# Performance work log

Measured on AMD Instinct MI355X. Metric: run time of the kernel, lower is better.

## Reference

```python
import jax, jax.numpy as jnp
import numpy as np
from jax import lax

NSTEPS = 4
STEPSIZE = 0.1


def setup_inputs() -> dict:
    key = jax.random.key(0)
    k1, k2, k3, k4 = jax.random.split(key, 4)
    B, N, D = 8, 40962, 40  # batch, n_patch, d_latent+d_ancillary
    H, D_DYN = 512, 32
    x = jax.random.normal(k1, (B, N, D), dtype=jnp.float32)
    # stencil: self + 3 neighbours per dual-mesh vertex
    nbrs = jax.random.randint(k2, (N, 3), 0, N, dtype=jnp.int32)
    index = jnp.concatenate([jnp.arange(N, dtype=jnp.int32)[:, None], nbrs], axis=1)  # (N,4)
    W1 = jax.random.normal(k3, (4, D, H), dtype=jnp.float32) * (1.0 / np.sqrt(4 * D))
    b1 = jnp.zeros((H,), dtype=jnp.float32)
    W2 = jax.random.normal(k4, (H, D_DYN), dtype=jnp.float32) * (1.0 / np.sqrt(H))
    b2 = jnp.zeros((D_DYN,), dtype=jnp.float32)
    return {"x": x, "index": index, "W1": W1, "b1": b1, "W2": W2, "b2": b2}


def interaction_model(z, W1, b1, W2, b2):
    # z: (B, N, 4, D) -> (B, N, d_dyn); MLP over flattened 4-vertex stencil
    h = jax.nn.gelu(jnp.einsum('bnkd,kdh->bnh', z, W1) + b1)
    return h @ W2 + b2


def reference(x, index, W1, b1, W2, b2):
    D = x.shape[-1]
    d_dyn = W2.shape[-1]

    def step(x, _):
        z = x[:, index, :]                       # (B, N, 4, D) gather of 4-neighbour stencil
        fz = interaction_model(z, W1, b1, W2, b2)  # (B, N, d_dyn)
        dx = jnp.pad(fz, ((0, 0), (0, 0), (0, D - d_dyn)))  # ancillary channels untouched
        return x + STEPSIZE * dx, None

    x, _ = lax.scan(step, x, None, length=NSTEPS)
    return x
```

## Files before the change

### kernel.cpp

```cpp
#include <hip/hip_runtime.h>
#include <math.h>

constexpr int BB   = 8;
constexpr int NN   = 40962;
constexpr int DDIM = 40;
constexpr int HH   = 512;
constexpr int DDYN = 32;
constexpr float STEPSZ = 0.1f;

constexpr int TM   = 64;
constexpr int NTHR = 1024;
constexpr int ZS   = 168;

constexpr size_t X_ELEMS = (size_t)BB * NN * DDIM;
constexpr size_t X_BYTES = X_ELEMS * 4;
constexpr int W1P_ELEMS = 32 * 5 * 64 * 8;
constexpr int W2P_BYTES = 2 * 16 * 64 * 8;

constexpr int Z_BYTES = TM * ZS * 2;
constexpr int H_OFF   = Z_BYTES;
constexpr int H_BYTES = TM * HH;
constexpr int XS_OFF  = H_OFF + H_BYTES;
constexpr int LDS_TOT = XS_OFF + TM * DDIM * 4;

typedef __attribute__((ext_vector_type(8))) short short8;
typedef __attribute__((ext_vector_type(4))) float f32x4;

__device__ __forceinline__ unsigned short bf16_rne(float f) {
    unsigned int u = __float_as_uint(f);
    return (unsigned short)((u + 0x7FFFu + ((u >> 16) & 1u)) >> 16);
}

__device__ __forceinline__ unsigned int cvt_pk_bf16(float lo, float hi) {
    unsigned int r;
    asm("v_cvt_pk_bf16_f32 %0, %1, %2" : "=v"(r) : "v"(lo), "v"(hi));
    return r;
}

__device__ __forceinline__ float exp2_hw(float x) {
    float r;
    asm("v_exp_f32 %0, %1" : "=v"(r) : "v"(x));
    return r;
}

__device__ __forceinline__ unsigned char f32_to_fp8_sw(float f) {
    if (!(f == f)) return 0x7f;
    unsigned u = __float_as_uint(f);
    unsigned s = (u >> 24) & 0x80u;
    float a = fabsf(f);
    if (a >= 464.f) return (unsigned char)(s | 0x7e);
    int e = (int)((u >> 23) & 0xff) - 127;
    if (e < -6) {
        int q = (int)fminf(fmaxf(a * 512.0f + 0.5f, 0.f), 7.f);
        return (unsigned char)(s | q);
    }
    unsigned m = u & 0x7fffffu;
    unsigned keep = m >> 20, rest = m & 0xfffffu;
    keep += (rest > 0x80000u || (rest == 0x80000u && (keep & 1u))) ? 1u : 0u;
    if (keep == 8u) { keep = 0u; ++e; if (e > 8) return (unsigned char)(s | 0x7e); }
    return (unsigned char)(s | ((unsigned)(e + 7) << 3) | keep);
}

__device__ __forceinline__ unsigned int pk4_fp8(float a, float b, float c, float d) {
#if __has_builtin(__builtin_amdgcn_cvt_pk_fp8_f32)
    int r = __builtin_amdgcn_cvt_pk_fp8_f32(a, b, 0, false);
    r     = __builtin_amdgcn_cvt_pk_fp8_f32(c, d, r, true);
    return (unsigned int)r;
#else
    return (unsigned)f32_to_fp8_sw(a) | ((unsigned)f32_to_fp8_sw(b) << 8) |
           ((unsigned)f32_to_fp8_sw(c) << 16) | ((unsigned)f32_to_fp8_sw(d) << 24);
#endif
}

__device__ __forceinline__ f32x4 gelu4(f32x4 a) {
    float d0, d1, d2, d3;
    {
        float t0 = a[0] * fmaf(-0.10294357f, a[0] * a[0], -2.3022077f);
        float t1 = a[1] * fmaf(-0.10294357f, a[1] * a[1], -2.3022077f);
        float t2 = a[2] * fmaf(-0.10294357f, a[2] * a[2], -2.3022077f);
        float t3 = a[3] * fmaf(-0.10294357f, a[3] * a[3], -2.3022077f);
        d0 = 1.0f + exp2_hw(t0);
        d1 = 1.0f + exp2_hw(t1);
        d2 = 1.0f + exp2_hw(t2);
        d3 = 1.0f + exp2_hw(t3);
    }
    float r01 = __builtin_amdgcn_rcpf(d0 * d1);
    float r23 = __builtin_amdgcn_rcpf(d2 * d3);
    f32x4 g;
    g[0] = a[0] * d1 * r01;
    g[1] = a[1] * d0 * r01;
    g[2] = a[2] * d3 * r23;
    g[3] = a[3] * d2 * r23;
    return g;
}

__global__ __launch_bounds__(256) void pack_w1(const float* __restrict__ W1,
                                               unsigned short* __restrict__ W1p) {
    int t = blockIdx.x * 256 + threadIdx.x;
    if (t >= W1P_ELEMS) return;
    int j = t & 7, ln = (t >> 3) & 63, g = t >> 9;
    int kk = g % 5, mt = g / 5;
    int nl = ln & 15, q = ln >> 4;
    int k = kk * 32 + q * 8 + j, m = mt * 16 + nl;
    W1p[t] = bf16_rne(W1[(size_t)k * HH + m]);
}
__global__ __launch_bounds__(256) void pack_w2_fp8(const float* __restrict__ W2,
                                                   unsigned char* __restrict__ W2p) {
    int t = blockIdx.x * 256 + threadIdx.x;
    if (t >= W2P_BYTES) return;
    int j = t & 7, ln = (t >> 3) & 63, g = t >> 9;
    int kk = g & 15, jt = g >> 4;
    int nl = ln & 15, q = ln >> 4;
    int k = kk * 32 + q * 8 + j, m = jt * 16 + nl;
    float v = W2[(size_t)k * DDYN + m];
#if __has_builtin(__builtin_amdgcn_cvt_pk_fp8_f32)
    W2p[t] = (unsigned char)(__builtin_amdgcn_cvt_pk_fp8_f32(v, v, 0, false) & 0xff);
#else
    W2p[t] = f32_to_fp8_sw(v);
#endif
}

__global__ __launch_bounds__(NTHR, 8) void step_mfma(
    const float* __restrict__ xsrc, float* __restrict__ xdst,
    const int* __restrict__ index,
    const unsigned short* __restrict__ W1p, const float* __restrict__ b1,
    const unsigned char* __restrict__ W2p, const float* __restrict__ b2,
    int write_static)
{
    __shared__ alignas(16) unsigned char smem[LDS_TOT];
    unsigned short* z = (unsigned short*)smem;
    unsigned char*  h = smem + H_OFF;
    float* xself = (float*)(smem + XS_OFF);

    const int tid = threadIdx.x;
    const int w   = tid >> 6;
    const int ln  = tid & 63;
    const int nl  = ln & 15;
    const int q   = ln >> 4;
    const int n0  = blockIdx.x * TM;
    const int b   = blockIdx.y;
    const size_t xbase = (size_t)b * NN * DDIM;

    if (n0 + TM <= NN) {
        for (int e = tid; e < TM * 4 * 10; e += NTHR) {
            int m = e / 40, r = e - m * 40;
            int k = r / 10, qq = r - k * 10;
            int nb = index[(n0 + m) * 4 + k];
            float4 v = ((const float4*)(xsrc + xbase + (size_t)nb * DDIM))[qq];
            unsigned lo = cvt_pk_bf16(v.x, v.y);
            unsigned hi = cvt_pk_bf16(v.z, v.w);
            *(uint2*)(z + m * ZS + k * 40 + qq * 4) = make_uint2(lo, hi);
            if (k == 0) {
                int c = (qq < 8) ? (qq ^ (m & 7)) : qq;
                *(float4*)(xself + m * 40 + c * 4) = v;
            }
        }
    } else {
        for (int e = tid; e < TM * 4 * 10; e += NTHR) {
            int m = e / 40, r = e - m * 40;
            int k = r / 10, qq = r - k * 10;
            unsigned lo = 0, hi = 0;
            int n = n0 + m;
            float4 v = make_float4(0.f, 0.f, 0.f, 0.f);
            if (n < NN) {
                int nb = index[n * 4 + k];
                v = ((const float4*)(xsrc + xbase + (size_t)nb * DDIM))[qq];
                lo = cvt_pk_bf16(v.x, v.y);
                hi = cvt_pk_bf16(v.z, v.w);
            }
            *(uint2*)(z + m * ZS + k * 40 + qq * 4) = make_uint2(lo, hi);
            if (k == 0) {
                int c = (qq < 8) ? (qq ^ (m & 7)) : qq;
                *(float4*)(xself + m * 40 + c * 4) = v;
            }
        }
    }
    const unsigned short* w1b = W1p + ((size_t)(w * 2) * 5) * 512 + ln * 8;
    short8 pf0 = *(const short8*)(w1b);
    short8 pf1 = *(const short8*)(w1b + 5 * 512);
    __syncthreads();

    f32x4 acc[2][4];
    #pragma unroll
    for (int i = 0; i < 2; ++i) {
        float4 bv = *(const float4*)(b1 + (w * 2 + i) * 16 + q * 4);
        f32x4 a; a[0] = bv.x; a[1] = bv.y; a[2] = bv.z; a[3] = bv.w;
        #pragma unroll
        for (int nt = 0; nt < 4; ++nt) acc[i][nt] = a;
    }
    short8 afr0 = pf0, afr1 = pf1;
    #pragma unroll
    for (int kk = 0; kk < 5; ++kk) {
        short8 na0, na1;
        if (kk < 4) {
            na0 = *(const short8*)(w1b + (kk + 1) * 512);
            na1 = *(const short8*)(w1b + (5 + kk + 1) * 512);
        }
        #pragma unroll
        for (int nt = 0; nt < 4; ++nt) {
            short8 bfr = *(const short8*)(z + (nt * 16 + nl) * ZS + kk * 32 + q * 8);
            acc[0][nt] = __builtin_amdgcn_mfma_f32_16x16x32_bf16(afr0, bfr, acc[0][nt], 0, 0, 0);
            acc[1][nt] = __builtin_amdgcn_mfma_f32_16x16x32_bf16(afr1, bfr, acc[1][nt], 0, 0, 0);
        }
        afr0 = na0; afr1 = na1;
    }

    #pragma unroll
    for (int i = 0; i < 2; ++i) {
        const int hid  = (w * 2 + i) * 16 + q * 4;
        const int sub8 = hid >> 3;
        const int o4   = (q & 1) << 2;
        #pragma unroll
        for (int nt = 0; nt < 4; ++nt) {
            f32x4 g = gelu4(acc[i][nt]);
            unsigned int p = pk4_fp8(g[0], g[1], g[2], g[3]);
            int node = nt * 16 + nl;
            *(unsigned int*)(h + node * 512 + ((sub8 ^ (node & 15)) << 3) + o4) = p;
        }
    }

    long long pa0 = 0, pa1 = 0;
    if (w < 4) {
        __builtin_memcpy(&pa0, W2p + (size_t)((0 * 64 + ln) * 8), 8);
        __builtin_memcpy(&pa1, W2p + (size_t)(((16) * 64 + ln) * 8), 8);
    }
    __syncthreads();

    if (w < 4) {
        const int hrow = w * 16 + nl;
        f32x4 acc2[2];
        #pragma unroll
        for (int jt = 0; jt < 2; ++jt) {
            float4 bv = *(const float4*)(b2 + jt * 16 + q * 4);
            acc2[jt][0] = bv.x; acc2[jt][1] = bv.y; acc2[jt][2] = bv.z; acc2[jt][3] = bv.w;
        }
        long long a0 = pa0, a1 = pa1;
        #pragma unroll
        for (int kg = 0; kg < 16; ++kg) {
            long long n0a, n1a;
            if (kg < 15) {
                __builtin_memcpy(&n0a, W2p + (size_t)(((kg + 1) * 64 + ln) * 8), 8);
                __builtin_memcpy(&n1a, W2p + (size_t)(((16 + kg + 1) * 64 + ln) * 8), 8);
            }
            long long bfr;
            __builtin_memcpy(&bfr, h + hrow * 512 + (((kg * 4 + q) ^ (hrow & 15)) << 3), 8);
            acc2[0] = __builtin_amdgcn_mfma_f32_16x16x32_fp8_fp8(a0, bfr, acc2[0], 0, 0, 0);
            acc2[1] = __builtin_amdgcn_mfma_f32_16x16x32_fp8_fp8(a1, bfr, acc2[1], 0, 0, 0);
            a0 = n0a; a1 = n1a;
        }
        int n = n0 + hrow;
        if (n < NN) {
            #pragma unroll
            for (int jt = 0; jt < 2; ++jt) {
                int c = (jt * 4 + q) ^ (hrow & 7);
                float4 s = *(const float4*)(xself + hrow * 40 + c * 4);
                float4 o;
                o.x = fmaf(STEPSZ, acc2[jt][0], s.x);
                o.y = fmaf(STEPSZ, acc2[jt][1], s.y);
                o.z = fmaf(STEPSZ, acc2[jt][2], s.z);
                o.w = fmaf(STEPSZ, acc2[jt][3], s.w);
                *(float4*)(xdst + xbase + (size_t)n * DDIM + jt * 16 + q * 4) = o;
            }
        }
    } else if (write_static) {
        int t2 = tid - 256;
        if (t2 < TM * 2) {
            int m = t2 >> 1, qq = 8 + (t2 & 1);
            int n = n0 + m;
            if (n < NN) {
                float4 v = *(const float4*)(xself + m * 40 + qq * 4);
                *(float4*)(xdst + xbase + (size_t)n * DDIM + qq * 4) = v;
            }
        }
    }
}

constexpr int FTM = 16;
__device__ __forceinline__ float gelu_f(float x) {
    float t = x * fmaf(-0.10294357f, x * x, -2.3022077f);
    return x * __builtin_amdgcn_rcpf(1.0f + exp2_hw(t));
}
__global__ __launch_bounds__(256) void step_f32(
    const float* __restrict__ xsrc, float* __restrict__ xdst,
    const int* __restrict__ index,
    const float* __restrict__ W1, const float* __restrict__ b1,
    const float* __restrict__ W2, const float* __restrict__ b2)
{
    __shared__ float z_lds[FTM][160];
    __shared__ float h_lds[FTM][HH];
    __shared__ float fz_lds[FTM][DDYN];
    const int tid = threadIdx.x, tile = blockIdx.x, b = blockIdx.y;
    const int n0 = tile * FTM;
    const int nvalid = min(FTM, NN - n0);
    for (int e = tid; e < FTM * 4 * 10; e += 256) {
        int m = e / 40, r = e % 40, k = r / 10, qq = r % 10;
        float4 v = make_float4(0.f, 0.f, 0.f, 0.f);
        int n = n0 + m;
        if (n < NN) {
            int nb = index[n * 4 + k];
            v = ((const float4*)(xsrc + ((size_t)b * NN + nb) * DDIM))[qq];
        }
        ((float4*)&z_lds[m][k * DDIM])[qq] = v;
    }
    __syncthreads();
    const int c0 = 2 * tid;
    float2 acc[FTM];
    {
        float bx = b1[c0], by = b1[c0 + 1];
        #pragma unroll
        for (int m = 0; m < FTM; ++m) { acc[m].x = bx; acc[m].y = by; }
    }
    for (int kd = 0; kd < 160; kd += 4) {
        float2 w0 = *(const float2*)(W1 + (size_t)(kd + 0) * HH + c0);
        float2 w1 = *(const float2*)(W1 + (size_t)(kd + 1) * HH + c0);
        float2 w2 = *(const float2*)(W1 + (size_t)(kd + 2) * HH + c0);
        float2 w3 = *(const float2*)(W1 + (size_t)(kd + 3) * HH + c0);
        #pragma unroll
        for (int m = 0; m < FTM; ++m) {
            float4 zv = *(const float4*)&z_lds[m][kd];
            acc[m].x = fmaf(zv.x, w0.x, acc[m].x); acc[m].y = fmaf(zv.x, w0.y, acc[m].y);
            acc[m].x = fmaf(zv.y, w1.x, acc[m].x); acc[m].y = fmaf(zv.y, w1.y, acc[m].y);
            acc[m].x = fmaf(zv.z, w2.x, acc[m].x); acc[m].y = fmaf(zv.z, w2.y, acc[m].y);
            acc[m].x = fmaf(zv.w, w3.x, acc[m].x); acc[m].y = fmaf(zv.w, w3.y, acc[m].y);
        }
    }
    #pragma unroll
    for (int m = 0; m < FTM; ++m) {
        h_lds[m][c0]     = gelu_f(acc[m].x);
        h_lds[m][c0 + 1] = gelu_f(acc[m].y);
    }
    __syncthreads();
    {
        const int j = tid & 31, mg = tid >> 5;
        float a0 = b2[j], a1 = a0;
        for (int c = 0; c < HH; c += 4) {
            float wa = W2[(size_t)(c + 0) * DDYN + j];
            float wb = W2[(size_t)(c + 1) * DDYN + j];
            float wc = W2[(size_t)(c + 2) * DDYN + j];
            float wd = W2[(size_t)(c + 3) * DDYN + j];
            float4 h0 = *(const float4*)&h_lds[mg][c];
            float4 h1 = *(const float4*)&h_lds[mg + 8][c];
            a0 = fmaf(h0.x, wa, a0); a0 = fmaf(h0.y, wb, a0);
            a0 = fmaf(h0.z, wc, a0); a0 = fmaf(h0.w, wd, a0);
            a1 = fmaf(h1.x, wa, a1); a1 = fmaf(h1.y, wb, a1);
            a1 = fmaf(h1.z, wc, a1); a1 = fmaf(h1.w, wd, a1);
        }
        fz_lds[mg][j] = a0; fz_lds[mg + 8][j] = a1;
    }
    __syncthreads();
    const size_t base = ((size_t)b * NN + n0) * (size_t)DDIM;
    for (int e = tid; e < nvalid * DDIM; e += 256) {
        int m = e / DDIM, d = e % DDIM;
        float v = xsrc[base + e];
        if (d < DDYN) v = fmaf(STEPSZ, fz_lds[m][d], v);
        xdst[base + e] = v;
    }
}

extern "C" void kernel_launch(void* const* d_in, const int* in_sizes, int n_in,
                              void* d_out, int out_size, void* d_ws, size_t ws_size,
                              hipStream_t stream) {
    const float* x   = (const float*)d_in[0];
    const int*   idx = (const int*)  d_in[1];
    const float* W1  = (const float*)d_in[2];
    const float* b1  = (const float*)d_in[3];
    const float* W2  = (const float*)d_in[4];
    const float* b2  = (const float*)d_in[5];
    float* out  = (float*)d_out;
    float* xbuf = (float*)d_ws;

    const size_t need = X_BYTES + (size_t)W1P_ELEMS * 2 + W2P_BYTES;
    if (ws_size >= need) {
        unsigned short* W1p = (unsigned short*)((char*)d_ws + X_BYTES);
        unsigned char*  W2p = (unsigned char*)(W1p + W1P_ELEMS);
        pack_w1<<<(W1P_ELEMS + 255) / 256, 256, 0, stream>>>(W1, W1p);
        pack_w2_fp8<<<(W2P_BYTES + 255) / 256, 256, 0, stream>>>(W2, W2p);
        dim3 grid((NN + TM - 1) / TM, BB), block(NTHR);
        step_mfma<<<grid, block, 0, stream>>>(x,    xbuf, idx, W1p, b1, W2p, b2, 1);
        step_mfma<<<grid, block, 0, stream>>>(xbuf, out,  idx, W1p, b1, W2p, b2, 1);
        step_mfma<<<grid, block, 0, stream>>>(out,  xbuf, idx, W1p, b1, W2p, b2, 0);
        step_mfma<<<grid, block, 0, stream>>>(xbuf, out,  idx, W1p, b1, W2p, b2, 0);
    } else {
        dim3 grid((NN + FTM - 1) / FTM, BB), block(256);
        step_f32<<<grid, block, 0, stream>>>(x,    xbuf, idx, W1, b1, W2, b2);
        step_f32<<<grid, block, 0, stream>>>(xbuf, out,  idx, W1, b1, W2, b2);
        step_f32<<<grid, block, 0, stream>>>(out,  xbuf, idx, W1, b1, W2, b2);
        step_f32<<<grid, block, 0, stream>>>(xbuf, out,  idx, W1, b1, W2, b2);
    }
}
```

Measured before the change: 655.4 us.

## Split second GEMM across all 16 waves with split-K reduction and coalesced stores

The second-layer FP8 MFMA work, previously done by only 4 of 16 waves, is spread over all waves by output tile, column tile and K-half, and the two K-halves are reduced through LDS. W2 fragments are prefetched into registers before the GELU epilogue, and the gather loop is unrolled into three explicit loads issued together. The result is written back into the x tile in LDS, and the full 40-channel rows are stored coalesced every step instead of skipping the static channels on later steps. This adds two extra barriers and more register pressure, and now rewrites the ancillary channels on all four steps.

```diff
diff --git a/kernel.cpp b/kernel.cpp
--- a/kernel.cpp
+++ b/kernel.cpp
@@ -124,13 +124,13 @@
     const float* __restrict__ xsrc, float* __restrict__ xdst,
     const int* __restrict__ index,
     const unsigned short* __restrict__ W1p, const float* __restrict__ b1,
-    const unsigned char* __restrict__ W2p, const float* __restrict__ b2,
-    int write_static)
+    const unsigned char* __restrict__ W2p, const float* __restrict__ b2)
 {
     __shared__ alignas(16) unsigned char smem[LDS_TOT];
     unsigned short* z = (unsigned short*)smem;
     unsigned char*  h = smem + H_OFF;
     float* xself = (float*)(smem + XS_OFF);
+    float* stg   = (float*)smem;
 
     const int tid = threadIdx.x;
     const int w   = tid >> 6;
@@ -141,19 +141,35 @@
     const int b   = blockIdx.y;
     const size_t xbase = (size_t)b * NN * DDIM;
 
+    const int nt2 = w & 3;
+    const int jt  = (w >> 2) & 1;
+    const int kh  = w >> 3;
+
     if (n0 + TM <= NN) {
-        for (int e = tid; e < TM * 4 * 10; e += NTHR) {
-            int m = e / 40, r = e - m * 40;
-            int k = r / 10, qq = r - k * 10;
-            int nb = index[(n0 + m) * 4 + k];
-            float4 v = ((const float4*)(xsrc + xbase + (size_t)nb * DDIM))[qq];
-            unsigned lo = cvt_pk_bf16(v.x, v.y);
-            unsigned hi = cvt_pk_bf16(v.z, v.w);
-            *(uint2*)(z + m * ZS + k * 40 + qq * 4) = make_uint2(lo, hi);
-            if (k == 0) {
-                int c = (qq < 8) ? (qq ^ (m & 7)) : qq;
-                *(float4*)(xself + m * 40 + c * 4) = v;
-            }
+        const int e0 = tid, e1 = tid + NTHR, e2 = tid + 2 * NTHR;
+        const bool has2 = (e2 < TM * 40);
+        int m0 = e0 / 40, r0 = e0 - m0 * 40, k0 = r0 / 10, q0 = r0 - k0 * 10;
+        int m1 = e1 / 40, r1 = e1 - m1 * 40, k1 = r1 / 10, q1 = r1 - k1 * 10;
+        int m2 = e2 / 40, r2 = e2 - m2 * 40, k2 = r2 / 10, q2 = r2 - k2 * 10;
+        int nb0 = index[(n0 + m0) * 4 + k0];
+        int nb1 = index[(n0 + m1) * 4 + k1];
+        int nb2 = has2 ? index[(n0 + m2) * 4 + k2] : nb1;
+        float4 v0 = ((const float4*)(xsrc + xbase + (size_t)nb0 * DDIM))[q0];
+        float4 v1 = ((const float4*)(xsrc + xbase + (size_t)nb1 * DDIM))[q1];
+        float4 v2 = ((const float4*)(xsrc + xbase + (size_t)nb2 * DDIM))[has2 ? q2 : q1];
+        *(uint2*)(z + m0 * ZS + k0 * 40 + q0 * 4) =
+            make_uint2(cvt_pk_bf16(v0.x, v0.y), cvt_pk_bf16(v0.z, v0.w));
+        if (k0 == 0) { int c = (q0 < 8) ? (q0 ^ (m0 & 7)) : q0;
+                       *(float4*)(xself + m0 * 40 + c * 4) = v0; }
+        *(uint2*)(z + m1 * ZS + k1 * 40 + q1 * 4) =
+            make_uint2(cvt_pk_bf16(v1.x, v1.y), cvt_pk_bf16(v1.z, v1.w));
+        if (k1 == 0) { int c = (q1 < 8) ? (q1 ^ (m1 & 7)) : q1;
+                       *(float4*)(xself + m1 * 40 + c * 4) = v1; }
+        if (has2) {
+            *(uint2*)(z + m2 * ZS + k2 * 40 + q2 * 4) =
+                make_uint2(cvt_pk_bf16(v2.x, v2.y), cvt_pk_bf16(v2.z, v2.w));
+            if (k2 == 0) { int c = (q2 < 8) ? (q2 ^ (m2 & 7)) : q2;
+                           *(float4*)(xself + m2 * 40 + c * 4) = v2; }
         }
     } else {
         for (int e = tid; e < TM * 4 * 10; e += NTHR) {
@@ -205,6 +221,11 @@
         afr0 = na0; afr1 = na1;
     }
 
+    long long wf[8];
+    #pragma unroll
+    for (int kk = 0; kk < 8; ++kk)
+        __builtin_memcpy(&wf[kk], W2p + (size_t)(((jt * 16 + kh * 8 + kk) * 64 + ln) * 8), 8);
+
     #pragma unroll
     for (int i = 0; i < 2; ++i) {
         const int hid  = (w * 2 + i) * 16 + q * 4;
@@ -218,59 +239,47 @@
             *(unsigned int*)(h + node * 512 + ((sub8 ^ (node & 15)) << 3) + o4) = p;
         }
     }
-
-    long long pa0 = 0, pa1 = 0;
-    if (w < 4) {
-        __builtin_memcpy(&pa0, W2p + (size_t)((0 * 64 + ln) * 8), 8);
-        __builtin_memcpy(&pa1, W2p + (size_t)(((16) * 64 + ln) * 8), 8);
-    }
-    __syncthreads();
-
-    if (w < 4) {
-        const int hrow = w * 16 + nl;
-        f32x4 acc2[2];
-        #pragma unroll
-        for (int jt = 0; jt < 2; ++jt) {
-            float4 bv = *(const float4*)(b2 + jt * 16 + q * 4);
-            acc2[jt][0] = bv.x; acc2[jt][1] = bv.y; acc2[jt][2] = bv.z; acc2[jt][3] = bv.w;
-        }
-        long long a0 = pa0, a1 = pa1;
-        #pragma unroll
-        for (int kg = 0; kg < 16; ++kg) {
-            long long n0a, n1a;
-            if (kg < 15) {
-                __builtin_memcpy(&n0a, W2p + (size_t)(((kg + 1) * 64 + ln) * 8), 8);
-                __builtin_memcpy(&n1a, W2p + (size_t)(((16 + kg + 1) * 64 + ln) * 8), 8);
-            }
-            long long bfr;
-            __builtin_memcpy(&bfr, h + hrow * 512 + (((kg * 4 + q) ^ (hrow & 15)) << 3), 8);
-            acc2[0] = __builtin_amdgcn_mfma_f32_16x16x32_fp8_fp8(a0, bfr, acc2[0], 0, 0, 0);
-            acc2[1] = __builtin_amdgcn_mfma_f32_16x16x32_fp8_fp8(a1, bfr, acc2[1], 0, 0, 0);
-            a0 = n0a; a1 = n1a;
-        }
-        int n = n0 + hrow;
+    __syncthreads();
+
+    const int hrow = nt2 * 16 + nl;
+    f32x4 acc2;
+    if (kh == 0) {
+        float4 bv = *(const float4*)(b2 + jt * 16 + q * 4);
+        acc2[0] = bv.x; acc2[1] = bv.y; acc2[2] = bv.z; acc2[3] = bv.w;
+    } else {
+        acc2[0] = acc2[1] = acc2[2] = acc2[3] = 0.f;
+    }
+    #pragma unroll
+    for (int kk = 0; kk < 8; ++kk) {
+        int kg = kh * 8 + kk;
+        long long bfr;
+        __builtin_memcpy(&bfr, h + hrow * 512 + (((kg * 4 + q) ^ (hrow & 15)) << 3), 8);
+        acc2 = __builtin_amdgcn_mfma_f32_16x16x32_fp8_fp8(wf[kk], bfr, acc2, 0, 0, 0);
+    }
+    if (kh == 1)
+        *(f32x4*)(stg + ((w - 8) * 64 + ln) * 4) = acc2;
+    __syncthreads();
+
+    if (kh == 0) {
+        f32x4 p = *(const f32x4*)(stg + (w * 64 + ln) * 4);
+        int c = (jt * 4 + q) ^ (hrow & 7);
+        float* xp = xself + hrow * 40 + c * 4;
+        float4 s = *(const float4*)xp;
+        s.x = fmaf(STEPSZ, acc2[0] + p[0], s.x);
+        s.y = fmaf(STEPSZ, acc2[1] + p[1], s.y);
+        s.z = fmaf(STEPSZ, acc2[2] + p[2], s.z);
+        s.w = fmaf(STEPSZ, acc2[3] + p[3], s.w);
+        *(float4*)xp = s;
+    }
+    __syncthreads();
+
+    if (tid < TM * 10) {
+        int m = tid / 10, p = tid - m * 10;
+        int n = n0 + m;
         if (n < NN) {
-            #pragma unroll
-            for (int jt = 0; jt < 2; ++jt) {
-                int c = (jt * 4 + q) ^ (hrow & 7);
-                float4 s = *(const float4*)(xself + hrow * 40 + c * 4);
-                float4 o;
-                o.x = fmaf(STEPSZ, acc2[jt][0], s.x);
-                o.y = fmaf(STEPSZ, acc2[jt][1], s.y);
-                o.z = fmaf(STEPSZ, acc2[jt][2], s.z);
-                o.w = fmaf(STEPSZ, acc2[jt][3], s.w);
-                *(float4*)(xdst + xbase + (size_t)n * DDIM + jt * 16 + q * 4) = o;
-            }
-        }
-    } else if (write_static) {
-        int t2 = tid - 256;
-        if (t2 < TM * 2) {
-            int m = t2 >> 1, qq = 8 + (t2 & 1);
-            int n = n0 + m;
-            if (n < NN) {
-                float4 v = *(const float4*)(xself + m * 40 + qq * 4);
-                *(float4*)(xdst + xbase + (size_t)n * DDIM + qq * 4) = v;
-            }
+            int c = (p < 8) ? (p ^ (m & 7)) : p;
+            float4 v = *(const float4*)(xself + m * 40 + c * 4);
+            *(float4*)(xdst + xbase + (size_t)n * DDIM + p * 4) = v;
         }
     }
 }
@@ -376,10 +385,10 @@
         pack_w1<<<(W1P_ELEMS + 255) / 256, 256, 0, stream>>>(W1, W1p);
         pack_w2_fp8<<<(W2P_BYTES + 255) / 256, 256, 0, stream>>>(W2, W2p);
         dim3 grid((NN + TM - 1) / TM, BB), block(NTHR);
-        step_mfma<<<grid, block, 0, stream>>>(x,    xbuf, idx, W1p, b1, W2p, b2, 1);
-        step_mfma<<<grid, block, 0, stream>>>(xbuf, out,  idx, W1p, b1, W2p, b2, 1);
-        step_mfma<<<grid, block, 0, stream>>>(out,  xbuf, idx, W1p, b1, W2p, b2, 0);
-        step_mfma<<<grid, block, 0, stream>>>(xbuf, out,  idx, W1p, b1, W2p, b2, 0);
+        step_mfma<<<grid, block, 0, stream>>>(x,    xbuf, idx, W1p, b1, W2p, b2);
+        step_mfma<<<grid, block, 0, stream>>>(xbuf, out,  idx, W1p, b1, W2p, b2);
+        step_mfma<<<grid, block, 0, stream>>>(out,  xbuf, idx, W1p, b1, W2p, b2);
+        step_mfma<<<grid, block, 0, stream>>>(xbuf, out,  idx, W1p, b1, W2p, b2);
     } else {
         dim3 grid((NN + FTM - 1) / FTM, BB), block(256);
         step_f32<<<grid, block, 0, stream>>>(x,    xbuf, idx, W1, b1, W2, b2);
```

After: 637.8 us. 1.03x faster.
